# Performance work log

Hardware: AMD Instinct MI355X
Metric: run time of the kernel (lower is better)

## Reference

```python
import jax, jax.numpy as jnp
import numpy as np

N_NODES = 100000
N_EDGES = 600000
IN_C, HID_C, OUT_C = 128, 128, 64


def setup_inputs() -> dict:
    key = jax.random.key(0)
    k1, k2, k3, k4 = jax.random.split(key, 4)
    x = jax.random.normal(k1, (N_NODES, IN_C), dtype=jnp.float32)
    edge_index = jax.random.randint(k2, (2, N_EDGES), 0, N_NODES, dtype=jnp.int64)
    # Glorot-ish init for linear weights
    W1 = jax.random.normal(k3, (IN_C, HID_C), dtype=jnp.float32) / np.sqrt(IN_C)
    b1 = jnp.zeros((HID_C,), dtype=jnp.float32)
    W2 = jax.random.normal(k4, (HID_C, OUT_C), dtype=jnp.float32) / np.sqrt(HID_C)
    b2 = jnp.zeros((OUT_C,), dtype=jnp.float32)
    prelu_a = jnp.full((1,), 0.25, dtype=jnp.float32)  # torch nn.PReLU default
    return {"x": x, "edge_index": edge_index, "W1": W1, "b1": b1,
            "W2": W2, "b2": b2, "prelu_a": prelu_a}


def _gcn_conv(x, src, dst, norm, W, b, num_nodes):
    # PyG GCNConv: h = x W; out[i] = sum_{(j->i)} norm_ji * h[j] + b
    h = x @ W                                   # [N, C_out]
    msg = h[src] * norm[:, None]                # [E', C_out] gather + scale
    out = jax.ops.segment_sum(msg, dst, num_segments=num_nodes)
    return out + b


def reference(x, edge_index, W1, b1, W2, b2, prelu_a):
    n = x.shape[0]
    # add self-loops
    loops = jnp.arange(n, dtype=edge_index.dtype)
    src = jnp.concatenate([edge_index[0], loops])
    dst = jnp.concatenate([edge_index[1], loops])
    # symmetric normalization deg^{-1/2}[src] * deg^{-1/2}[dst]
    deg = jax.ops.segment_sum(jnp.ones_like(dst, dtype=x.dtype), dst, num_segments=n)
    dinv = jnp.where(deg > 0, jax.lax.rsqrt(deg), 0.0)
    norm = dinv[src] * dinv[dst]
    # dropout p=0.0 -> identity
    h = _gcn_conv(x, src, dst, norm, W1, b1, n)
    h = jnp.where(h >= 0, h, prelu_a * h)       # PReLU (single shared parameter)
    out = _gcn_conv(h, src, dst, norm, W2, b2, n)
    return out
```

## Files before the change

kernel.cpp:

```cpp
#include <hip/hip_runtime.h>


typedef __attribute__((ext_vector_type(8))) short bf16x8;
typedef __attribute__((ext_vector_type(4))) float f32x4;

#define CAP 32

__device__ inline unsigned short f2bf(float f) {
    unsigned int b = __float_as_uint(f);
    b += 0x7FFFu + ((b >> 16) & 1u);
    return (unsigned short)(b >> 16);
}
__device__ inline float bflo(unsigned int u) { return __uint_as_float(u << 16); }
__device__ inline float bfhi(unsigned int u) { return __uint_as_float(u & 0xFFFF0000u); }

__global__ void k_pre(const float* __restrict__ W1, const float* __restrict__ W2,
                      unsigned short* __restrict__ Wt1, unsigned short* __restrict__ Wt2,
                      int* __restrict__ cnt, int n) {
    int i = blockIdx.x * blockDim.x + threadIdx.x;
    if (i < n) cnt[i] = 0;
    if (i < 128 * 128) {
        int nn = i >> 7, k = i & 127;
        Wt1[i] = f2bf(W1[k * 128 + nn]);
    } else if (i < 128 * 128 + 64 * 128) {
        int j = i - 128 * 128;
        int nn = j >> 7, k = j & 127;
        Wt2[j] = f2bf(W2[k * 64 + nn]);
    }
}

template <int BN, bool CVT, bool FILL>
__global__ __launch_bounds__(512) void k_gemm_mfma(
    const void* __restrict__ Asrc, const unsigned short* __restrict__ Wt,
    unsigned short* __restrict__ H, int n,
    const int* __restrict__ esrc, const int* __restrict__ edst,
    int* __restrict__ cnt, int* __restrict__ bucket, int e) {
    constexpr int PITCH = 136;
    __shared__ unsigned short Bs[BN * PITCH];
    const int tid = threadIdx.x;

    for (int q = tid; q < BN * 16; q += 512) {
        int row = q >> 4, c16 = q & 15;
        *(uint4*)(Bs + row * PITCH + c16 * 8) =
            *(const uint4*)(Wt + row * 128 + c16 * 8);
    }

    const int wave = tid >> 6, lane = tid & 63;
    const int ml = lane & 15;
    const int g = lane >> 4;
    const int stripe = blockIdx.x * 8 + wave;

    int ra = stripe * 16 + ml;
    if (ra >= n) ra = n - 1;

    bf16x8 af[4];
    if (CVT) {
        const float* A = (const float*)Asrc;
#pragma unroll
        for (int ks = 0; ks < 4; ++ks) {
            const float* p = A + (size_t)ra * 128 + ks * 32 + g * 8;
            float4 a0 = *(const float4*)p;
            float4 a1 = *(const float4*)(p + 4);
            uint4 pk;
            pk.x = (unsigned)f2bf(a0.x) | ((unsigned)f2bf(a0.y) << 16);
            pk.y = (unsigned)f2bf(a0.z) | ((unsigned)f2bf(a0.w) << 16);
            pk.z = (unsigned)f2bf(a1.x) | ((unsigned)f2bf(a1.y) << 16);
            pk.w = (unsigned)f2bf(a1.z) | ((unsigned)f2bf(a1.w) << 16);
            af[ks] = *(bf16x8*)&pk;
        }
    } else {
        const unsigned short* A = (const unsigned short*)Asrc;
#pragma unroll
        for (int ks = 0; ks < 4; ++ks)
            af[ks] = *(const bf16x8*)(A + (size_t)ra * 128 + ks * 32 + g * 8);
    }

    if (FILL) {
        for (int i = blockIdx.x * 512 + tid; i < e; i += gridDim.x * 512) {
            int d = edst[i];
            int s = esrc[i];
            int pos = atomicAdd(&cnt[d], 1);
            if (pos < CAP) bucket[(size_t)d * CAP + pos] = s;
        }
    }

    __syncthreads();

    constexpr int NCT = BN / 16;
    f32x4 acc[NCT];
#pragma unroll
    for (int ct = 0; ct < NCT; ++ct) acc[ct] = (f32x4){0.f, 0.f, 0.f, 0.f};

#pragma unroll
    for (int ks = 0; ks < 4; ++ks)
#pragma unroll
        for (int ct = 0; ct < NCT; ++ct) {
            bf16x8 b = *(const bf16x8*)(Bs + (size_t)(ct * 16 + ml) * PITCH + ks * 32 + g * 8);
            acc[ct] = __builtin_amdgcn_mfma_f32_16x16x32_bf16(af[ks], b, acc[ct], 0, 0, 0);
        }

#pragma unroll
    for (int ct = 0; ct < NCT; ++ct)
#pragma unroll
        for (int reg = 0; reg < 4; ++reg) {
            int r = stripe * 16 + g * 4 + reg;
            if (r < n) H[(size_t)r * BN + ct * 16 + ml] = f2bf(acc[ct][reg]);
        }
}

template <int COLS, bool PRELU_BF16_OUT>
__global__ void k_gather(const unsigned short* __restrict__ H,
                         const int* __restrict__ cnt, const int* __restrict__ bucket,
                         const float* __restrict__ b, void* __restrict__ outp,
                         const float* __restrict__ alpha_p, int n) {
    constexpr int NT = COLS / 8;
    constexpr int G = 256 / NT;
    const int tid = threadIdx.x;
    const int node = blockIdx.x * G + tid / NT;
    if (node >= n) return;
    const int c0 = (tid & (NT - 1)) * 8;

    int c = cnt[node];
    const float di = rsqrtf(1.0f + (float)c);
    if (c > CAP) c = CAP;

    float acc[8];
    {
        uint4 v = *(const uint4*)(H + (size_t)node * COLS + c0);
        float sl = di * di;
        acc[0] = bflo(v.x) * sl + b[c0 + 0];
        acc[1] = bfhi(v.x) * sl + b[c0 + 1];
        acc[2] = bflo(v.y) * sl + b[c0 + 2];
        acc[3] = bfhi(v.y) * sl + b[c0 + 3];
        acc[4] = bflo(v.z) * sl + b[c0 + 4];
        acc[5] = bfhi(v.z) * sl + b[c0 + 5];
        acc[6] = bflo(v.w) * sl + b[c0 + 6];
        acc[7] = bfhi(v.w) * sl + b[c0 + 7];
    }

    const int* bp = bucket + (size_t)node * CAP;
    const int nb4 = (c + 3) >> 2;
    for (int q = 0; q < nb4; ++q) {
        int4 idx = *(const int4*)(bp + q * 4);
        int base = q * 4;
        int s0 = idx.x;
        int s1 = (base + 1 < c) ? idx.y : s0;
        int s2 = (base + 2 < c) ? idx.z : s0;
        int s3 = (base + 3 < c) ? idx.w : s0;
        int cn0 = cnt[s0], cn1 = cnt[s1], cn2 = cnt[s2], cn3 = cnt[s3];
        uint4 v0 = *(const uint4*)(H + (size_t)s0 * COLS + c0);
        uint4 v1 = *(const uint4*)(H + (size_t)s1 * COLS + c0);
        uint4 v2 = *(const uint4*)(H + (size_t)s2 * COLS + c0);
        uint4 v3 = *(const uint4*)(H + (size_t)s3 * COLS + c0);
        float n0 = rsqrtf(1.0f + (float)cn0) * di;
        float n1 = (base + 1 < c) ? rsqrtf(1.0f + (float)cn1) * di : 0.0f;
        float n2 = (base + 2 < c) ? rsqrtf(1.0f + (float)cn2) * di : 0.0f;
        float n3 = (base + 3 < c) ? rsqrtf(1.0f + (float)cn3) * di : 0.0f;
        acc[0] += bflo(v0.x) * n0; acc[1] += bfhi(v0.x) * n0;
        acc[2] += bflo(v0.y) * n0; acc[3] += bfhi(v0.y) * n0;
        acc[4] += bflo(v0.z) * n0; acc[5] += bfhi(v0.z) * n0;
        acc[6] += bflo(v0.w) * n0; acc[7] += bfhi(v0.w) * n0;
        acc[0] += bflo(v1.x) * n1; acc[1] += bfhi(v1.x) * n1;
        acc[2] += bflo(v1.y) * n1; acc[3] += bfhi(v1.y) * n1;
        acc[4] += bflo(v1.z) * n1; acc[5] += bfhi(v1.z) * n1;
        acc[6] += bflo(v1.w) * n1; acc[7] += bfhi(v1.w) * n1;
        acc[0] += bflo(v2.x) * n2; acc[1] += bfhi(v2.x) * n2;
        acc[2] += bflo(v2.y) * n2; acc[3] += bfhi(v2.y) * n2;
        acc[4] += bflo(v2.z) * n2; acc[5] += bfhi(v2.z) * n2;
        acc[6] += bflo(v2.w) * n2; acc[7] += bfhi(v2.w) * n2;
        acc[0] += bflo(v3.x) * n3; acc[1] += bfhi(v3.x) * n3;
        acc[2] += bflo(v3.y) * n3; acc[3] += bfhi(v3.y) * n3;
        acc[4] += bflo(v3.z) * n3; acc[5] += bfhi(v3.z) * n3;
        acc[6] += bflo(v3.w) * n3; acc[7] += bfhi(v3.w) * n3;
    }

    if (PRELU_BF16_OUT) {
        float al = alpha_p[0];
        unsigned short o[8];
#pragma unroll
        for (int j = 0; j < 8; ++j) {
            float t = acc[j];
            t = (t >= 0.f) ? t : al * t;
            o[j] = f2bf(t);
        }
        uint4 pk;
        pk.x = (unsigned)o[0] | ((unsigned)o[1] << 16);
        pk.y = (unsigned)o[2] | ((unsigned)o[3] << 16);
        pk.z = (unsigned)o[4] | ((unsigned)o[5] << 16);
        pk.w = (unsigned)o[6] | ((unsigned)o[7] << 16);
        *(uint4*)((unsigned short*)outp + (size_t)node * COLS + c0) = pk;
    } else {
        float* out = (float*)outp;
        *(float4*)(out + (size_t)node * COLS + c0) =
            make_float4(acc[0], acc[1], acc[2], acc[3]);
        *(float4*)(out + (size_t)node * COLS + c0 + 4) =
            make_float4(acc[4], acc[5], acc[6], acc[7]);
    }
}

extern "C" void kernel_launch(void* const* d_in, const int* in_sizes, int n_in,
                              void* d_out, int out_size, void* d_ws, size_t ws_size,
                              hipStream_t stream) {
    const float* x  = (const float*)d_in[0];
    const int*   ei = (const int*)d_in[1];
    const float* W1 = (const float*)d_in[2];
    const float* b1 = (const float*)d_in[3];
    const float* W2 = (const float*)d_in[4];
    const float* b2 = (const float*)d_in[5];
    const float* pa = (const float*)d_in[6];
    float* out = (float*)d_out;

    const int n = in_sizes[0] / 128;
    const int e = in_sizes[1] / 2;
    const int* src = ei;
    const int* dst = ei + e;
    const int B = 256;

    unsigned short* h1  = (unsigned short*)d_ws;
    unsigned short* hp  = h1 + (size_t)n * 128;
    unsigned short* h2  = hp + (size_t)n * 128;
    unsigned short* Wt1 = h2 + (size_t)n * 64;
    unsigned short* Wt2 = Wt1 + 128 * 128;
    int* cnt     = (int*)(Wt2 + 64 * 128);
    int* bucket  = cnt + n;

    const int gblk = ((n + 15) / 16 + 7) / 8;

    k_pre<<<(n + B - 1) / B, B, 0, stream>>>(W1, W2, Wt1, Wt2, cnt, n);
    k_gemm_mfma<128, true, true><<<gblk, 512, 0, stream>>>(
        x, Wt1, h1, n, src, dst, cnt, bucket, e);
    k_gather<128, true><<<(n + 15) / 16, 256, 0, stream>>>(h1, cnt, bucket,
                                                           b1, hp, pa, n);
    k_gemm_mfma<64, false, false><<<gblk, 512, 0, stream>>>(
        hp, Wt2, h2, n, nullptr, nullptr, nullptr, nullptr, 0);
    k_gather<64, false><<<(n + 31) / 32, 256, 0, stream>>>(h2, cnt, bucket,
                                                           b2, out, nullptr, n);
}
```

Baseline: 197.6 us.

## Fuse layer-1 gather with layer-2 GEMM and split bucket fill across kernels

```diff
diff --git a/kernel.cpp b/kernel.cpp
--- a/kernel.cpp
+++ b/kernel.cpp
@@ -14,18 +14,32 @@
 __device__ inline float bflo(unsigned int u) { return __uint_as_float(u << 16); }
 __device__ inline float bfhi(unsigned int u) { return __uint_as_float(u & 0xFFFF0000u); }
 
-__global__ void k_pre(const float* __restrict__ W1, const float* __restrict__ W2,
-                      unsigned short* __restrict__ Wt1, unsigned short* __restrict__ Wt2,
-                      int* __restrict__ cnt, int n) {
-    int i = blockIdx.x * blockDim.x + threadIdx.x;
-    if (i < n) cnt[i] = 0;
-    if (i < 128 * 128) {
-        int nn = i >> 7, k = i & 127;
-        Wt1[i] = f2bf(W1[k * 128 + nn]);
-    } else if (i < 128 * 128 + 64 * 128) {
-        int j = i - 128 * 128;
+__global__ __launch_bounds__(512) void k_pre(
+    const float* __restrict__ W1, const float* __restrict__ W2,
+    unsigned short* __restrict__ Wt1, unsigned short* __restrict__ Wt2,
+    const int* __restrict__ esrc, const int* __restrict__ edst,
+    int* __restrict__ cnt, int* __restrict__ bucket, int ea) {
+    const int t = blockIdx.x * 512 + threadIdx.x;
+    if (t < 128 * 128) {
+        int nn = t >> 7, k = t & 127;
+        Wt1[t] = f2bf(W1[k * 128 + nn]);
+    } else if (t < 128 * 128 + 64 * 128) {
+        int j = t - 128 * 128;
         int nn = j >> 7, k = j & 127;
         Wt2[j] = f2bf(W2[k * 64 + nn]);
+    }
+    const int4* s4 = (const int4*)esrc;
+    const int4* d4 = (const int4*)edst;
+    for (int i = t; i < (ea >> 2); i += gridDim.x * 512) {
+        int4 s = s4[i], d = d4[i];
+        int p0 = atomicAdd(&cnt[d.x], 1);
+        int p1 = atomicAdd(&cnt[d.y], 1);
+        int p2 = atomicAdd(&cnt[d.z], 1);
+        int p3 = atomicAdd(&cnt[d.w], 1);
+        if (p0 < CAP) bucket[(size_t)d.x * CAP + p0] = s.x;
+        if (p1 < CAP) bucket[(size_t)d.y * CAP + p1] = s.y;
+        if (p2 < CAP) bucket[(size_t)d.z * CAP + p2] = s.z;
+        if (p3 < CAP) bucket[(size_t)d.w * CAP + p3] = s.w;
     }
 }
 
@@ -34,7 +48,7 @@
     const void* __restrict__ Asrc, const unsigned short* __restrict__ Wt,
     unsigned short* __restrict__ H, int n,
     const int* __restrict__ esrc, const int* __restrict__ edst,
-    int* __restrict__ cnt, int* __restrict__ bucket, int e) {
+    int* __restrict__ cnt, int* __restrict__ bucket, int e, int ea) {
     constexpr int PITCH = 136;
     __shared__ unsigned short Bs[BN * PITCH];
     const int tid = threadIdx.x;
@@ -76,7 +90,7 @@
     }
 
     if (FILL) {
-        for (int i = blockIdx.x * 512 + tid; i < e; i += gridDim.x * 512) {
+        for (int i = ea + blockIdx.x * 512 + tid; i < e; i += gridDim.x * 512) {
             int d = edst[i];
             int s = esrc[i];
             int pos = atomicAdd(&cnt[d], 1);
@@ -106,6 +120,124 @@
             int r = stripe * 16 + g * 4 + reg;
             if (r < n) H[(size_t)r * BN + ct * 16 + ml] = f2bf(acc[ct][reg]);
         }
+}
+
+__global__ __launch_bounds__(512) void k_gather_gemm(
+    const unsigned short* __restrict__ H,
+    const int* __restrict__ cnt, const int* __restrict__ bucket,
+    const float* __restrict__ b1, const float* __restrict__ alpha_p,
+    const unsigned short* __restrict__ Wt2,
+    unsigned short* __restrict__ H2,
+    int n) {
+    constexpr int PITCH = 136;
+    __shared__ unsigned short As[32 * PITCH];
+    __shared__ unsigned short Bs[64 * PITCH];
+    const int tid = threadIdx.x;
+
+    for (int q = tid; q < 64 * 16; q += 512) {
+        int row = q >> 4, c16 = q & 15;
+        *(uint4*)(Bs + row * PITCH + c16 * 8) =
+            *(const uint4*)(Wt2 + row * 128 + c16 * 8);
+    }
+
+    const int node = blockIdx.x * 32 + tid / 16;
+    const int c0 = (tid & 15) * 8;
+    const int lr = tid / 16;
+
+    if (node < n) {
+        int c = cnt[node];
+        const float di = rsqrtf(1.0f + (float)c);
+        if (c > CAP) c = CAP;
+
+        float acc[8];
+        {
+            uint4 v = *(const uint4*)(H + (size_t)node * 128 + c0);
+            float sl = di * di;
+            acc[0] = bflo(v.x) * sl + b1[c0 + 0];
+            acc[1] = bfhi(v.x) * sl + b1[c0 + 1];
+            acc[2] = bflo(v.y) * sl + b1[c0 + 2];
+            acc[3] = bfhi(v.y) * sl + b1[c0 + 3];
+            acc[4] = bflo(v.z) * sl + b1[c0 + 4];
+            acc[5] = bfhi(v.z) * sl + b1[c0 + 5];
+            acc[6] = bflo(v.w) * sl + b1[c0 + 6];
+            acc[7] = bfhi(v.w) * sl + b1[c0 + 7];
+        }
+
+        const int* bp = bucket + (size_t)node * CAP;
+        const int nb4 = (c + 3) >> 2;
+        for (int q = 0; q < nb4; ++q) {
+            int4 idx = *(const int4*)(bp + q * 4);
+            int base = q * 4;
+            int s0 = idx.x;
+            int s1 = (base + 1 < c) ? idx.y : s0;
+            int s2 = (base + 2 < c) ? idx.z : s0;
+            int s3 = (base + 3 < c) ? idx.w : s0;
+            int cn0 = cnt[s0], cn1 = cnt[s1], cn2 = cnt[s2], cn3 = cnt[s3];
+            uint4 v0 = *(const uint4*)(H + (size_t)s0 * 128 + c0);
+            uint4 v1 = *(const uint4*)(H + (size_t)s1 * 128 + c0);
+            uint4 v2 = *(const uint4*)(H + (size_t)s2 * 128 + c0);
+            uint4 v3 = *(const uint4*)(H + (size_t)s3 * 128 + c0);
+            float n0 = rsqrtf(1.0f + (float)cn0) * di;
+            float n1 = (base + 1 < c) ? rsqrtf(1.0f + (float)cn1) * di : 0.0f;
+            float n2 = (base + 2 < c) ? rsqrtf(1.0f + (float)cn2) * di : 0.0f;
+            float n3 = (base + 3 < c) ? rsqrtf(1.0f + (float)cn3) * di : 0.0f;
+            acc[0] += bflo(v0.x) * n0; acc[1] += bfhi(v0.x) * n0;
+            acc[2] += bflo(v0.y) * n0; acc[3] += bfhi(v0.y) * n0;
+            acc[4] += bflo(v0.z) * n0; acc[5] += bfhi(v0.z) * n0;
+            acc[6] += bflo(v0.w) * n0; acc[7] += bfhi(v0.w) * n0;
+            acc[0] += bflo(v1.x) * n1; acc[1] += bfhi(v1.x) * n1;
+            acc[2] += bflo(v1.y) * n1; acc[3] += bfhi(v1.y) * n1;
+            acc[4] += bflo(v1.z) * n1; acc[5] += bfhi(v1.z) * n1;
+            acc[6] += bflo(v1.w) * n1; acc[7] += bfhi(v1.w) * n1;
+            acc[0] += bflo(v2.x) * n2; acc[1] += bfhi(v2.x) * n2;
+            acc[2] += bflo(v2.y) * n2; acc[3] += bfhi(v2.y) * n2;
+            acc[4] += bflo(v2.z) * n2; acc[5] += bfhi(v2.z) * n2;
+            acc[6] += bflo(v2.w) * n2; acc[7] += bfhi(v2.w) * n2;
+            acc[0] += bflo(v3.x) * n3; acc[1] += bfhi(v3.x) * n3;
+            acc[2] += bflo(v3.y) * n3; acc[3] += bfhi(v3.y) * n3;
+            acc[4] += bflo(v3.z) * n3; acc[5] += bfhi(v3.z) * n3;
+            acc[6] += bflo(v3.w) * n3; acc[7] += bfhi(v3.w) * n3;
+        }
+
+        float al = alpha_p[0];
+        unsigned short o[8];
+#pragma unroll
+        for (int j = 0; j < 8; ++j) {
+            float t = acc[j];
+            t = (t >= 0.f) ? t : al * t;
+            o[j] = f2bf(t);
+        }
+        uint4 pk;
+        pk.x = (unsigned)o[0] | ((unsigned)o[1] << 16);
+        pk.y = (unsigned)o[2] | ((unsigned)o[3] << 16);
+        pk.z = (unsigned)o[4] | ((unsigned)o[5] << 16);
+        pk.w = (unsigned)o[6] | ((unsigned)o[7] << 16);
+        *(uint4*)(As + lr * PITCH + c0) = pk;
+    }
+    __syncthreads();
+
+    const int wave = tid >> 6, lane = tid & 63;
+    const int ml = lane & 15, g = lane >> 4;
+    const int stripe = wave >> 2;
+    const int ct = wave & 3;
+
+    bf16x8 af[4];
+#pragma unroll
+    for (int ks = 0; ks < 4; ++ks)
+        af[ks] = *(const bf16x8*)(As + (size_t)(stripe * 16 + ml) * PITCH + ks * 32 + g * 8);
+
+    f32x4 acc2 = (f32x4){0.f, 0.f, 0.f, 0.f};
+#pragma unroll
+    for (int ks = 0; ks < 4; ++ks) {
+        bf16x8 bb = *(const bf16x8*)(Bs + (size_t)(ct * 16 + ml) * PITCH + ks * 32 + g * 8);
+        acc2 = __builtin_amdgcn_mfma_f32_16x16x32_bf16(af[ks], bb, acc2, 0, 0, 0);
+    }
+
+#pragma unroll
+    for (int reg = 0; reg < 4; ++reg) {
+        int r = blockIdx.x * 32 + stripe * 16 + g * 4 + reg;
+        if (r < n) H2[(size_t)r * 64 + ct * 16 + ml] = f2bf(acc2[reg]);
+    }
 }
 
 template <int COLS, bool PRELU_BF16_OUT>
@@ -214,25 +346,27 @@
     const int e = in_sizes[1] / 2;
     const int* src = ei;
     const int* dst = ei + e;
-    const int B = 256;
 
     unsigned short* h1  = (unsigned short*)d_ws;
-    unsigned short* hp  = h1 + (size_t)n * 128;
-    unsigned short* h2  = hp + (size_t)n * 128;
+    unsigned short* h2  = h1 + (size_t)n * 128;
     unsigned short* Wt1 = h2 + (size_t)n * 64;
     unsigned short* Wt2 = Wt1 + 128 * 128;
     int* cnt     = (int*)(Wt2 + 64 * 128);
     int* bucket  = cnt + n;
 
+    int EA = (int)(((long long)e * 7) / 10) & ~3;
+    if ((e & 3) != 0) EA = 0;
+
     const int gblk = ((n + 15) / 16 + 7) / 8;
-
-    k_pre<<<(n + B - 1) / B, B, 0, stream>>>(W1, W2, Wt1, Wt2, cnt, n);
+    int pblk = (EA / 4 + 511) / 512;
+    if (pblk < 48) pblk = 48;
+
+    hipMemsetAsync(cnt, 0, (size_t)n * sizeof(int), stream);
+    k_pre<<<pblk, 512, 0, stream>>>(W1, W2, Wt1, Wt2, src, dst, cnt, bucket, EA);
     k_gemm_mfma<128, true, true><<<gblk, 512, 0, stream>>>(
-        x, Wt1, h1, n, src, dst, cnt, bucket, e);
-    k_gather<128, true><<<(n + 15) / 16, 256, 0, stream>>>(h1, cnt, bucket,
-                                                           b1, hp, pa, n);
-    k_gemm_mfma<64, false, false><<<gblk, 512, 0, stream>>>(
-        hp, Wt2, h2, n, nullptr, nullptr, nullptr, nullptr, 0);
+        x, Wt1, h1, n, src, dst, cnt, bucket, e, EA);
+    k_gather_gemm<<<(n + 31) / 32, 512, 0, stream>>>(h1, cnt, bucket, b1, pa,
+                                                     Wt2, h2, n);
     k_gather<64, false><<<(n + 31) / 32, 256, 0, stream>>>(h2, cnt, bucket,
                                                            b2, out, nullptr, n);
 }
```

Result: faster. 190.3 us (-3.7%).
